# Optimization experiments

Hardware: AMD Instinct MI355X
Metric: run time of the kernel (lower is better)

The kernel has to match this reference:

```python
import jax, jax.numpy as jnp
import numpy as np

N, E, D, DE, H = 50000, 400000, 128, 64, 8
EPS = 1e-5
SLOPE = 0.2


def setup_inputs() -> dict:
    key = jax.random.key(0)
    ks = jax.random.split(key, 16)

    def lin(k, fan_in, fan_out):
        return (jax.random.normal(k, (fan_in, fan_out), jnp.float32) / np.sqrt(fan_in)).astype(jnp.float32)

    return {
        "node_features": jax.random.normal(ks[0], (N, D), jnp.float32),
        "edge_features": jax.random.normal(ks[1], (E, DE), jnp.float32),
        "Wn": lin(ks[2], D, D), "bn": jnp.zeros((D,), jnp.float32),
        "Wq": lin(ks[3], D, D), "bq": jnp.zeros((D,), jnp.float32),
        "Wk": lin(ks[4], D, D), "bk": jnp.zeros((D,), jnp.float32),
        "Wv": lin(ks[5], D, D), "bv": jnp.zeros((D,), jnp.float32),
        "We": lin(ks[6], DE, D), "be": jnp.zeros((D,), jnp.float32),
        "A1": lin(ks[7], 3 * D, D), "b1": jnp.zeros((D,), jnp.float32),
        "A2": lin(ks[8], D, H), "b2": jnp.zeros((H,), jnp.float32),
        "gamma": jnp.ones((D,), jnp.float32),
        "beta": jnp.zeros((D,), jnp.float32),
        "edge_index": jax.random.randint(ks[9], (2, E), 0, N, dtype=jnp.int32),
    }


def reference(node_features, edge_features, Wn, bn, Wq, bq, Wk, bk, Wv, bv,
              We, be, A1, b1, A2, b2, gamma, beta, edge_index):
    num_nodes = node_features.shape[0]
    h = node_features @ Wn + bn                      # [N, D]
    q = node_features @ Wq + bq                      # [N, D]
    k = node_features @ Wk + bk                      # [N, D]
    v = node_features @ Wv + bv                      # [N, D]
    eh = edge_features @ We + be                     # [E, D]

    src, tgt = edge_index[0], edge_index[1]
    attn_in = jnp.concatenate([q[src], k[tgt], eh], axis=-1)   # [E, 3D]
    hmid = jax.nn.leaky_relu(attn_in @ A1 + b1, SLOPE)          # [E, D]
    scores = jax.nn.leaky_relu(hmid @ A2 + b2, SLOPE)           # [E, H]
    w = jax.nn.softmax(scores.mean(axis=-1), axis=0)            # global softmax over edges, [E]

    # scatter-add: output[src] += w * v[tgt]
    out = jax.ops.segment_sum(w[:, None] * v[tgt], src, num_segments=num_nodes)  # [N, D]

    y = h + out                                       # dropout = identity (eval)
    mu = y.mean(axis=-1, keepdims=True)
    var = y.var(axis=-1, keepdims=True)
    return gamma * (y - mu) / jnp.sqrt(var + EPS) + beta
```

## Files before the change

kernel.cpp:

```cpp
#include <hip/hip_runtime.h>

#define D 128
#define DE 64
#define SLOPE 0.2f
#define EPS 1e-5f

typedef float f32x4 __attribute__((ext_vector_type(4)));
typedef short bf16x8 __attribute__((ext_vector_type(8)));

__device__ __forceinline__ float lrelu(float x) { return x > 0.f ? x : SLOPE * x; }

__device__ __forceinline__ unsigned short f2bf(float x) {
  union { float f; unsigned u; } c; c.f = x;
  unsigned r = c.u + 0x7FFFu + ((c.u >> 16) & 1u);
  return (unsigned short)(r >> 16);
}
__device__ __forceinline__ float bf2f(unsigned short u) {
  return __uint_as_float(((unsigned)u) << 16);
}

__global__ __launch_bounds__(128) void fold_pack(
    const float* __restrict__ Wq, const float* __restrict__ Wk,
    const float* __restrict__ We, const float* __restrict__ A1,
    const float* __restrict__ bq, const float* __restrict__ bk,
    const float* __restrict__ be, const float* __restrict__ b1,
    const float* __restrict__ Wn, const float* __restrict__ Wv,
    unsigned short* __restrict__ AfqT, unsigned short* __restrict__ AfkT,
    unsigned short* __restrict__ AfeT, float* __restrict__ bfold,
    unsigned short* __restrict__ WnT, unsigned short* __restrict__ WvT) {
  int r = blockIdx.x;
  int j = threadIdx.x;
  if (r < 128) {
    float acc = 0.f;
    for (int t = 0; t < 128; ++t) acc += Wq[r * 128 + t] * A1[t * 128 + j];
    AfqT[j * 128 + r] = f2bf(acc);
  } else if (r < 256) {
    int k = r - 128;
    float acc = 0.f;
    for (int t = 0; t < 128; ++t) acc += Wk[k * 128 + t] * A1[(128 + t) * 128 + j];
    AfkT[j * 128 + k] = f2bf(acc);
  } else if (r < 320) {
    int k = r - 256;
    float acc = 0.f;
    for (int t = 0; t < 128; ++t) acc += We[k * 128 + t] * A1[(256 + t) * 128 + j];
    AfeT[j * 64 + k] = f2bf(acc);
  } else if (r == 320) {
    float acc = b1[j];
    for (int t = 0; t < 128; ++t) {
      acc += bq[t] * A1[t * 128 + j];
      acc += bk[t] * A1[(128 + t) * 128 + j];
      acc += be[t] * A1[(256 + t) * 128 + j];
    }
    bfold[j] = acc;
  } else if (r < 449) {
    int c = r - 321;
    WnT[c * 128 + j] = f2bf(Wn[j * 128 + c]);
  } else {
    int c = r - 449;
    WvT[c * 128 + j] = f2bf(Wv[j * 128 + c]);
  }
}

__global__ __launch_bounds__(256) void cvt_to_bf16(
    const float* __restrict__ X, unsigned short* __restrict__ Xb, int n4) {
  int i = blockIdx.x * 256 + threadIdx.x;
  if (i < n4) {
    float4 f = ((const float4*)X)[i];
    union { unsigned short us[4]; uint2 v; } u;
    u.us[0] = f2bf(f.x); u.us[1] = f2bf(f.y);
    u.us[2] = f2bf(f.z); u.us[3] = f2bf(f.w);
    ((uint2*)Xb)[i] = u.v;
  }
}

__global__ __launch_bounds__(256, 2) void node_gemm_mfma(
    const unsigned short* __restrict__ Xb, const unsigned short* __restrict__ WnT,
    const unsigned short* __restrict__ WvT, const unsigned short* __restrict__ AfqT,
    const unsigned short* __restrict__ AfkT, const float* __restrict__ bn,
    const float* __restrict__ bv, float* __restrict__ h, float* __restrict__ v,
    unsigned short* __restrict__ q2p, unsigned short* __restrict__ k2p, int Nn) {
  __shared__ unsigned short As[256 * 40];
  __shared__ unsigned short Bs[128 * 40];
  __shared__ float bS[128];
  const unsigned short* WT;
  const float* bb = nullptr;
  float* O = nullptr;
  unsigned short* Ob = nullptr;
  switch (blockIdx.y) {
    case 0: WT = WnT; bb = bn; O = h; break;
    case 1: WT = WvT; bb = bv; O = v; break;
    case 2: WT = AfqT; Ob = q2p; break;
    default: WT = AfkT; Ob = k2p; break;
  }
  const int t = threadIdx.x;
  if (t < 128) bS[t] = bb ? bb[t] : 0.f;
  const int seg = t & 3, arow = t >> 2;
  const int m0 = blockIdx.x * 256;
  int rIdx[4];
#pragma unroll
  for (int l = 0; l < 4; ++l) rIdx[l] = min(m0 + arow + 64 * l, Nn - 1);
  uint4 avA[4], avB[2];
#pragma unroll
  for (int l = 0; l < 4; ++l)
    avA[l] = *(const uint4*)(Xb + (size_t)rIdx[l] * 128 + seg * 8);
#pragma unroll
  for (int l = 0; l < 2; ++l)
    avB[l] = *(const uint4*)(WT + (arow + 64 * l) * 128 + seg * 8);
  f32x4 acc[4][8];
#pragma unroll
  for (int mt = 0; mt < 4; ++mt)
#pragma unroll
    for (int nt = 0; nt < 8; ++nt) acc[mt][nt] = (f32x4)(0.f);
  const int lane = t & 63, wv = t >> 6, l15 = lane & 15, quad = lane >> 4;
  for (int ch = 0; ch < 4; ++ch) {
#pragma unroll
    for (int l = 0; l < 4; ++l)
      *(uint4*)&As[(arow + 64 * l) * 40 + seg * 8] = avA[l];
#pragma unroll
    for (int l = 0; l < 2; ++l)
      *(uint4*)&Bs[(arow + 64 * l) * 40 + seg * 8] = avB[l];
    __syncthreads();
    if (ch < 3) {
      int o = (ch + 1) * 32 + seg * 8;
#pragma unroll
      for (int l = 0; l < 4; ++l)
        avA[l] = *(const uint4*)(Xb + (size_t)rIdx[l] * 128 + o);
#pragma unroll
      for (int l = 0; l < 2; ++l)
        avB[l] = *(const uint4*)(WT + (arow + 64 * l) * 128 + o);
    }
    bf16x8 af[4];
#pragma unroll
    for (int mt = 0; mt < 4; ++mt)
      af[mt] = *(const bf16x8*)&As[(wv * 64 + mt * 16 + l15) * 40 + quad * 8];
#pragma unroll
    for (int nt = 0; nt < 8; ++nt) {
      bf16x8 bfr = *(const bf16x8*)&Bs[(nt * 16 + l15) * 40 + quad * 8];
#pragma unroll
      for (int mt = 0; mt < 4; ++mt)
        acc[mt][nt] =
            __builtin_amdgcn_mfma_f32_16x16x32_bf16(af[mt], bfr, acc[mt][nt], 0, 0, 0);
    }
    __syncthreads();
  }
#pragma unroll
  for (int mt = 0; mt < 4; ++mt) {
    int rowb = m0 + wv * 64 + mt * 16 + quad * 4;
#pragma unroll
    for (int nt = 0; nt < 8; ++nt) {
      int col = nt * 16 + l15;
      float b = bS[col];
#pragma unroll
      for (int r = 0; r < 4; ++r) {
        int rg = rowb + r;
        if (rg < Nn) {
          if (O) O[(size_t)rg * 128 + col] = acc[mt][nt][r] + b;
          else   Ob[(size_t)rg * 128 + l15 * 8 + nt] = f2bf(acc[mt][nt][r]);
        }
      }
    }
  }
}

__global__ __launch_bounds__(256, 2) void edge_fused2(
    const float* __restrict__ EF, const unsigned short* __restrict__ AfeT,
    const float* __restrict__ bfold, const float* __restrict__ A2,
    const float* __restrict__ b2, const unsigned short* __restrict__ q2p,
    const unsigned short* __restrict__ k2p, const int* __restrict__ src,
    const int* __restrict__ tgt, float* __restrict__ s_out, int E) {
  __shared__ unsigned short As[256 * 40];
  __shared__ unsigned short Bs[128 * 40];
  __shared__ float A2s[128 * 9];
  __shared__ float bfS[128];
  __shared__ float b2s[8];
  __shared__ int sIdxS[256], sIdxT[256];
  const int t = threadIdx.x;
  const int e0 = blockIdx.x * 256;
  {
    int ec = min(e0 + t, E - 1);
    sIdxS[t] = src[ec];
    sIdxT[t] = tgt[ec];
    if (t < 128) bfS[t] = bfold[t];
    if (t < 8) b2s[t] = b2[t];
#pragma unroll
    for (int l = 0; l < 4; ++l) {
      int i = t + l * 256;
      A2s[(i >> 3) * 9 + (i & 7)] = A2[i];
    }
  }
  const int seg = t & 3, arow = t >> 2;
  int ecl[4];
#pragma unroll
  for (int l = 0; l < 4; ++l) ecl[l] = min(e0 + arow + 64 * l, E - 1);
  uint4 avA[4], avB[2];
#pragma unroll
  for (int l = 0; l < 4; ++l) {
    const float* p = EF + (size_t)ecl[l] * 64 + seg * 8;
    float4 f0 = *(const float4*)p;
    float4 f1 = *(const float4*)(p + 4);
    union { unsigned short us[8]; uint4 v; } u;
    u.us[0] = f2bf(f0.x); u.us[1] = f2bf(f0.y);
    u.us[2] = f2bf(f0.z); u.us[3] = f2bf(f0.w);
    u.us[4] = f2bf(f1.x); u.us[5] = f2bf(f1.y);
    u.us[6] = f2bf(f1.z); u.us[7] = f2bf(f1.w);
    avA[l] = u.v;
  }
#pragma unroll
  for (int l = 0; l < 2; ++l)
    avB[l] = *(const uint4*)(AfeT + (arow + 64 * l) * 64 + seg * 8);
  f32x4 acc[4][8];
#pragma unroll
  for (int mt = 0; mt < 4; ++mt)
#pragma unroll
    for (int nt = 0; nt < 8; ++nt) acc[mt][nt] = (f32x4)(0.f);
  const int lane = t & 63, wv = t >> 6, l15 = lane & 15, quad = lane >> 4;

#pragma unroll
  for (int ch = 0; ch < 2; ++ch) {
#pragma unroll
    for (int l = 0; l < 4; ++l)
      *(uint4*)&As[(arow + 64 * l) * 40 + seg * 8] = avA[l];
#pragma unroll
    for (int l = 0; l < 2; ++l)
      *(uint4*)&Bs[(arow + 64 * l) * 40 + seg * 8] = avB[l];
    __syncthreads();
    if (ch == 0) {
      int o = 32 + seg * 8;
#pragma unroll
      for (int l = 0; l < 4; ++l) {
        const float* p = EF + (size_t)ecl[l] * 64 + o;
        float4 f0 = *(const float4*)p;
        float4 f1 = *(const float4*)(p + 4);
        union { unsigned short us[8]; uint4 v; } u;
        u.us[0] = f2bf(f0.x); u.us[1] = f2bf(f0.y);
        u.us[2] = f2bf(f0.z); u.us[3] = f2bf(f0.w);
        u.us[4] = f2bf(f1.x); u.us[5] = f2bf(f1.y);
        u.us[6] = f2bf(f1.z); u.us[7] = f2bf(f1.w);
        avA[l] = u.v;
      }
#pragma unroll
      for (int l = 0; l < 2; ++l)
        avB[l] = *(const uint4*)(AfeT + (arow + 64 * l) * 64 + o);
    }
    bf16x8 af[4];
#pragma unroll
    for (int mt = 0; mt < 4; ++mt)
      af[mt] = *(const bf16x8*)&As[(wv * 64 + mt * 16 + l15) * 40 + quad * 8];
#pragma unroll
    for (int nt = 0; nt < 8; ++nt) {
      bf16x8 bfr = *(const bf16x8*)&Bs[(nt * 16 + l15) * 40 + quad * 8];
#pragma unroll
      for (int mt = 0; mt < 4; ++mt)
        acc[mt][nt] =
            __builtin_amdgcn_mfma_f32_16x16x32_bf16(af[mt], bfr, acc[mt][nt], 0, 0, 0);
    }
    if (ch == 0) __syncthreads();
  }

  float bfv[8];
#pragma unroll
  for (int nt = 0; nt < 8; ++nt) bfv[nt] = bfS[nt * 16 + l15];
#pragma unroll
  for (int mt = 0; mt < 4; ++mt) {
#pragma unroll
    for (int r = 0; r < 4; ++r) {
      int erow = wv * 64 + mt * 16 + quad * 4 + r;
      int si = sIdxS[erow], ti = sIdxT[erow];
      uint4 qv = *(const uint4*)(q2p + (size_t)si * 128 + l15 * 8);
      uint4 kv = *(const uint4*)(k2p + (size_t)ti * 128 + l15 * 8);
      const unsigned short* qs = (const unsigned short*)&qv;
      const unsigned short* ks = (const unsigned short*)&kv;
#pragma unroll
      for (int nt = 0; nt < 8; ++nt)
        acc[mt][nt][r] =
            lrelu(acc[mt][nt][r] + bf2f(qs[nt]) + bf2f(ks[nt]) + bfv[nt]);
    }
  }
  float tacc[4][4];
#pragma unroll
  for (int mt = 0; mt < 4; ++mt)
#pragma unroll
    for (int r = 0; r < 4; ++r) tacc[mt][r] = 0.f;
  for (int hh = 0; hh < 8; ++hh) {
    float a2v[8];
#pragma unroll
    for (int nt = 0; nt < 8; ++nt) a2v[nt] = A2s[nt * 144 + l15 * 9 + hh];
    float b2h = b2s[hh];
#pragma unroll
    for (int mt = 0; mt < 4; ++mt)
#pragma unroll
      for (int r = 0; r < 4; ++r) {
        float p = 0.f;
#pragma unroll
        for (int nt = 0; nt < 8; ++nt) p += acc[mt][nt][r] * a2v[nt];
        p += __shfl_xor(p, 1);
        p += __shfl_xor(p, 2);
        p += __shfl_xor(p, 4);
        p += __shfl_xor(p, 8);
        tacc[mt][r] += lrelu(p + b2h);
      }
  }
  if (l15 == 0) {
#pragma unroll
    for (int mt = 0; mt < 4; ++mt)
#pragma unroll
      for (int r = 0; r < 4; ++r) {
        int e = e0 + wv * 64 + mt * 16 + quad * 4 + r;
        if (e < E) s_out[e] = tacc[mt][r] * 0.125f;
      }
  }
}

__global__ __launch_bounds__(256) void softmax_partial(
    const float* __restrict__ s, int E, float2* __restrict__ part) {
  __shared__ float mS[256], sS[256];
  int tid = threadIdx.x;
  float m = -1e30f, sum = 0.f;
  for (int i = blockIdx.x * 256 + tid; i < E; i += gridDim.x * 256) {
    float x = s[i];
    if (x > m) {
      sum = sum * __expf(m - x) + 1.f;
      m = x;
    } else {
      sum += __expf(x - m);
    }
  }
  mS[tid] = m;
  sS[tid] = sum;
  __syncthreads();
  for (int off = 128; off > 0; off >>= 1) {
    if (tid < off) {
      float m1 = mS[tid], s1 = sS[tid];
      float m2 = mS[tid + off], s2 = sS[tid + off];
      float M = fmaxf(m1, m2);
      mS[tid] = M;
      sS[tid] = s1 * __expf(m1 - M) + s2 * __expf(m2 - M);
    }
    __syncthreads();
  }
  if (tid == 0) part[blockIdx.x] = make_float2(mS[0], sS[0]);
}

__global__ __launch_bounds__(256) void softmax_final(
    const float2* __restrict__ part, int nPart, float* __restrict__ MS) {
  __shared__ float mS[256], sS[256];
  int tid = threadIdx.x;
  float m = -1e30f, sum = 0.f;
  for (int i = tid; i < nPart; i += 256) {
    float2 p = part[i];
    float M = fmaxf(m, p.x);
    sum = sum * __expf(m - M) + p.y * __expf(p.x - M);
    m = M;
  }
  mS[tid] = m;
  sS[tid] = sum;
  __syncthreads();
  for (int off = 128; off > 0; off >>= 1) {
    if (tid < off) {
      float m1 = mS[tid], s1 = sS[tid];
      float m2 = mS[tid + off], s2 = sS[tid + off];
      float M = fmaxf(m1, m2);
      mS[tid] = M;
      sS[tid] = s1 * __expf(m1 - M) + s2 * __expf(m2 - M);
    }
    __syncthreads();
  }
  if (tid == 0) {
    MS[0] = mS[0];
    MS[1] = 1.f / sS[0];
  }
}

__global__ __launch_bounds__(256) void count_deg(const int* __restrict__ src,
                                                 int* __restrict__ deg, int E) {
  int e = blockIdx.x * 256 + threadIdx.x;
  if (e < E) atomicAdd(&deg[src[e]], 1);
}

__global__ __launch_bounds__(256) void scan1(const int* __restrict__ deg,
                                             int* __restrict__ incl,
                                             int* __restrict__ bsum, int N) {
  __shared__ int sh[256];
  int tid = threadIdx.x;
  int i = blockIdx.x * 256 + tid;
  sh[tid] = (i < N) ? deg[i] : 0;
  __syncthreads();
  for (int off = 1; off < 256; off <<= 1) {
    int tv = (tid >= off) ? sh[tid - off] : 0;
    __syncthreads();
    sh[tid] += tv;
    __syncthreads();
  }
  if (i < N) incl[i] = sh[tid];
  if (tid == 255) bsum[blockIdx.x] = sh[255];
}

__global__ __launch_bounds__(256) void scan2(int* __restrict__ bsum, int nb) {
  __shared__ int sh[256];
  int tid = threadIdx.x;
  sh[tid] = (tid < nb) ? bsum[tid] : 0;
  __syncthreads();
  for (int off = 1; off < 256; off <<= 1) {
    int tv = (tid >= off) ? sh[tid - off] : 0;
    __syncthreads();
    sh[tid] += tv;
    __syncthreads();
  }
  if (tid < nb) bsum[tid] = sh[tid];
}

__global__ __launch_bounds__(256) void scan3(const int* __restrict__ deg,
                                             const int* __restrict__ incl,
                                             const int* __restrict__ bsum,
                                             int* __restrict__ offs,
                                             int* __restrict__ cursor, int N,
                                             int E) {
  int i = blockIdx.x * 256 + threadIdx.x;
  if (i >= N) return;
  int base = (blockIdx.x > 0) ? bsum[blockIdx.x - 1] : 0;
  int ex = incl[i] - deg[i] + base;
  offs[i] = ex;
  cursor[i] = ex;
  if (i == N - 1) offs[N] = E;
}

__global__ __launch_bounds__(256) void fill_csr(
    const int* __restrict__ src, const int* __restrict__ tgt,
    const float* __restrict__ s, int* __restrict__ cursor,
    int2* __restrict__ cwt, int E) {
  int e = blockIdx.x * 256 + threadIdx.x;
  if (e >= E) return;
  int s_ = src[e];
  int j = atomicAdd(&cursor[s_], 1);
  cwt[j] = make_int2(tgt[e], __float_as_int(s[e]));
}

__global__ __launch_bounds__(256) void gather_ln(
    const int* __restrict__ offs, const int2* __restrict__ cwt,
    const float* __restrict__ v, const float* __restrict__ MS,
    const float* __restrict__ gamma, const float* __restrict__ beta,
    float* __restrict__ y, int N) {
  int tid = threadIdx.x;
  int n = blockIdx.x * 4 + (tid >> 6);
  if (n >= N) return;
  int lane = tid & 63;
  float M = MS[0], inv = MS[1];
  int beg = offs[n], end = offs[n + 1];
  float a0 = 0.f, a1 = 0.f;
  int j = beg;
  for (; j + 1 < end; j += 2) {
    int2 p0 = cwt[j], p1 = cwt[j + 1];
    float w0 = __expf(__int_as_float(p0.y) - M) * inv;
    float w1 = __expf(__int_as_float(p1.y) - M) * inv;
    float2 v0 = *(const float2*)(v + (size_t)p0.x * 128 + lane * 2);
    float2 v1 = *(const float2*)(v + (size_t)p1.x * 128 + lane * 2);
    a0 += w0 * v0.x + w1 * v1.x;
    a1 += w0 * v0.y + w1 * v1.y;
  }
  if (j < end) {
    int2 p = cwt[j];
    float w = __expf(__int_as_float(p.y) - M) * inv;
    float2 vv = *(const float2*)(v + (size_t)p.x * 128 + lane * 2);
    a0 += w * vv.x;
    a1 += w * vv.y;
  }
  size_t base = (size_t)n * 128 + lane * 2;
  float2 hv = *(const float2*)(y + base);
  float y0 = hv.x + a0, y1 = hv.y + a1;
  float sum = y0 + y1, ssq = y0 * y0 + y1 * y1;
#pragma unroll
  for (int off = 1; off < 64; off <<= 1) {
    sum += __shfl_xor(sum, off);
    ssq += __shfl_xor(ssq, off);
  }
  float mu = sum * (1.f / 128.f);
  float var = ssq * (1.f / 128.f) - mu * mu;
  float rstd = rsqrtf(var + EPS);
  float2 g = *(const float2*)(gamma + lane * 2);
  float2 bt = *(const float2*)(beta + lane * 2);
  float2 out;
  out.x = g.x * (y0 - mu) * rstd + bt.x;
  out.y = g.y * (y1 - mu) * rstd + bt.y;
  *(float2*)(y + base) = out;
}

extern "C" void kernel_launch(void* const* d_in, const int* in_sizes, int n_in,
                              void* d_out, int out_size, void* d_ws,
                              size_t ws_size, hipStream_t stream) {
  const float* X  = (const float*)d_in[0];
  const float* EF = (const float*)d_in[1];
  const float* Wn = (const float*)d_in[2];
  const float* bn = (const float*)d_in[3];
  const float* Wq = (const float*)d_in[4];
  const float* bq = (const float*)d_in[5];
  const float* Wk = (const float*)d_in[6];
  const float* bk = (const float*)d_in[7];
  const float* Wv = (const float*)d_in[8];
  const float* bv = (const float*)d_in[9];
  const float* We = (const float*)d_in[10];
  const float* be = (const float*)d_in[11];
  const float* A1 = (const float*)d_in[12];
  const float* b1 = (const float*)d_in[13];
  const float* A2 = (const float*)d_in[14];
  const float* b2 = (const float*)d_in[15];
  const float* gamma = (const float*)d_in[16];
  const float* beta  = (const float*)d_in[17];
  const int* ei = (const int*)d_in[18];

  int N = in_sizes[0] / D;
  int E = in_sizes[1] / DE;
  const int* src = ei;
  const int* tgt = ei + E;

  float* h = (float*)d_out;
  float* ws = (float*)d_ws;
  float* v     = ws;
  float* sbuf  = v + (size_t)N * D;
  float2* part = (float2*)(sbuf + E);
  float* MS    = (float*)(part + 1024);
  float* bfold = MS + 4;
  unsigned short* Xb   = (unsigned short*)(bfold + 128);
  unsigned short* q2p  = Xb + (size_t)N * D;
  unsigned short* k2p  = q2p + (size_t)N * D;
  unsigned short* AfqT = k2p + (size_t)N * D;
  unsigned short* AfkT = AfqT + 128 * 128;
  unsigned short* AfeT = AfkT + 128 * 128;
  unsigned short* WnT  = AfeT + 128 * 64;
  unsigned short* WvT  = WnT + 128 * 128;
  int* deg    = (int*)(WvT + 128 * 128);
  int* incl   = deg + N;
  int* bsum   = incl + N;
  int* cursor = bsum + 256;
  int* offs   = cursor + N;
  int2* cwt   = (int2*)(offs + N + 2);

  int nbScan = (N + 255) / 256;

  hipMemsetAsync(deg, 0, (size_t)N * sizeof(int), stream);
  fold_pack<<<577, 128, 0, stream>>>(Wq, Wk, We, A1, bq, bk, be, b1, Wn, Wv,
                                     AfqT, AfkT, AfeT, bfold, WnT, WvT);
  cvt_to_bf16<<<(N * D / 4 + 255) / 256, 256, 0, stream>>>(X, Xb, N * D / 4);
  count_deg<<<(E + 255) / 256, 256, 0, stream>>>(src, deg, E);
  scan1<<<nbScan, 256, 0, stream>>>(deg, incl, bsum, N);
  scan2<<<1, 256, 0, stream>>>(bsum, nbScan);
  scan3<<<nbScan, 256, 0, stream>>>(deg, incl, bsum, offs, cursor, N, E);
  node_gemm_mfma<<<dim3((N + 255) / 256, 4), 256, 0, stream>>>(
      Xb, WnT, WvT, AfqT, AfkT, bn, bv, h, v, q2p, k2p, N);
  edge_fused2<<<(E + 255) / 256, 256, 0, stream>>>(EF, AfeT, bfold, A2, b2,
                                                   q2p, k2p, src, tgt, sbuf, E);
  softmax_partial<<<1024, 256, 0, stream>>>(sbuf, E, part);
  softmax_final<<<1, 256, 0, stream>>>(part, 1024, MS);
  fill_csr<<<(E + 255) / 256, 256, 0, stream>>>(src, tgt, sbuf, cursor, cwt, E);
  gather_ln<<<(N + 3) / 4, 256, 0, stream>>>(offs, cwt, v, MS, gamma, beta, h,
                                             N);
}
```

Baseline: 436.8 us.

## Store v in bf16, fuse degree count into convert, prefetch q/k gathers

Three changes land together. The v projection is now written as bf16, which halves the bytes gather_ln reads in its random per-edge gather, at the cost of lower precision in the aggregation. The degree-count atomics are folded into the bf16 conversion kernel, removing one launch. In the edge kernel, src/tgt indices are held in registers and the q/k row gathers are double-buffered across m-tiles so load latency overlaps the score math, which costs extra registers.

```diff
diff --git a/kernel.cpp b/kernel.cpp
--- a/kernel.cpp
+++ b/kernel.cpp
@@ -7,16 +7,17 @@
 
 typedef float f32x4 __attribute__((ext_vector_type(4)));
 typedef short bf16x8 __attribute__((ext_vector_type(8)));
+typedef unsigned short ushort;
 
 __device__ __forceinline__ float lrelu(float x) { return x > 0.f ? x : SLOPE * x; }
 
-__device__ __forceinline__ unsigned short f2bf(float x) {
+__device__ __forceinline__ ushort f2bf(float x) {
   union { float f; unsigned u; } c; c.f = x;
   unsigned r = c.u + 0x7FFFu + ((c.u >> 16) & 1u);
-  return (unsigned short)(r >> 16);
-}
-__device__ __forceinline__ float bf2f(unsigned short u) {
-  return __uint_as_float(((unsigned)u) << 16);
+  return (ushort)(r >> 16);
+}
+__device__ __forceinline__ float bf2f(unsigned u) {
+  return __uint_as_float(u << 16);
 }
 
 __global__ __launch_bounds__(128) void fold_pack(
@@ -25,9 +26,9 @@
     const float* __restrict__ bq, const float* __restrict__ bk,
     const float* __restrict__ be, const float* __restrict__ b1,
     const float* __restrict__ Wn, const float* __restrict__ Wv,
-    unsigned short* __restrict__ AfqT, unsigned short* __restrict__ AfkT,
-    unsigned short* __restrict__ AfeT, float* __restrict__ bfold,
-    unsigned short* __restrict__ WnT, unsigned short* __restrict__ WvT) {
+    ushort* __restrict__ AfqT, ushort* __restrict__ AfkT,
+    ushort* __restrict__ AfeT, float* __restrict__ bfold,
+    ushort* __restrict__ WnT, ushort* __restrict__ WvT) {
   int r = blockIdx.x;
   int j = threadIdx.x;
   if (r < 128) {
@@ -61,36 +62,40 @@
   }
 }
 
-__global__ __launch_bounds__(256) void cvt_to_bf16(
-    const float* __restrict__ X, unsigned short* __restrict__ Xb, int n4) {
+__global__ __launch_bounds__(256) void cvt_count(
+    const float* __restrict__ X, ushort* __restrict__ Xb, int n4,
+    const int* __restrict__ src, int* __restrict__ deg, int E) {
   int i = blockIdx.x * 256 + threadIdx.x;
   if (i < n4) {
     float4 f = ((const float4*)X)[i];
-    union { unsigned short us[4]; uint2 v; } u;
+    union { ushort us[4]; uint2 v; } u;
     u.us[0] = f2bf(f.x); u.us[1] = f2bf(f.y);
     u.us[2] = f2bf(f.z); u.us[3] = f2bf(f.w);
     ((uint2*)Xb)[i] = u.v;
   }
+  if (i < E) atomicAdd(&deg[src[i]], 1);
 }
 
 __global__ __launch_bounds__(256, 2) void node_gemm_mfma(
-    const unsigned short* __restrict__ Xb, const unsigned short* __restrict__ WnT,
-    const unsigned short* __restrict__ WvT, const unsigned short* __restrict__ AfqT,
-    const unsigned short* __restrict__ AfkT, const float* __restrict__ bn,
-    const float* __restrict__ bv, float* __restrict__ h, float* __restrict__ v,
-    unsigned short* __restrict__ q2p, unsigned short* __restrict__ k2p, int Nn) {
-  __shared__ unsigned short As[256 * 40];
-  __shared__ unsigned short Bs[128 * 40];
+    const ushort* __restrict__ Xb, const ushort* __restrict__ WnT,
+    const ushort* __restrict__ WvT, const ushort* __restrict__ AfqT,
+    const ushort* __restrict__ AfkT, const float* __restrict__ bn,
+    const float* __restrict__ bv, float* __restrict__ h,
+    ushort* __restrict__ vb, ushort* __restrict__ q2p,
+    ushort* __restrict__ k2p, int Nn) {
+  __shared__ ushort As[256 * 40];
+  __shared__ ushort Bs[128 * 40];
   __shared__ float bS[128];
-  const unsigned short* WT;
+  const ushort* WT;
   const float* bb = nullptr;
   float* O = nullptr;
-  unsigned short* Ob = nullptr;
+  ushort* Ob = nullptr;
+  int mode;
   switch (blockIdx.y) {
-    case 0: WT = WnT; bb = bn; O = h; break;
-    case 1: WT = WvT; bb = bv; O = v; break;
-    case 2: WT = AfqT; Ob = q2p; break;
-    default: WT = AfkT; Ob = k2p; break;
+    case 0: WT = WnT; bb = bn; O = h; mode = 0; break;
+    case 1: WT = WvT; bb = bv; Ob = vb; mode = 1; break;
+    case 2: WT = AfqT; Ob = q2p; mode = 2; break;
+    default: WT = AfkT; Ob = k2p; mode = 2; break;
   }
   const int t = threadIdx.x;
   if (t < 128) bS[t] = bb ? bb[t] : 0.f;
@@ -154,32 +159,40 @@
       for (int r = 0; r < 4; ++r) {
         int rg = rowb + r;
         if (rg < Nn) {
-          if (O) O[(size_t)rg * 128 + col] = acc[mt][nt][r] + b;
-          else   Ob[(size_t)rg * 128 + l15 * 8 + nt] = f2bf(acc[mt][nt][r]);
+          if (mode == 0)      O[(size_t)rg * 128 + col] = acc[mt][nt][r] + b;
+          else if (mode == 1) Ob[(size_t)rg * 128 + col] = f2bf(acc[mt][nt][r] + b);
+          else                Ob[(size_t)rg * 128 + l15 * 8 + nt] = f2bf(acc[mt][nt][r]);
         }
       }
     }
   }
 }
 
-__global__ __launch_bounds__(256, 2) void edge_fused2(
-    const float* __restrict__ EF, const unsigned short* __restrict__ AfeT,
+__global__ __launch_bounds__(256, 2) void edge_fused3(
+    const float* __restrict__ EF, const ushort* __restrict__ AfeT,
     const float* __restrict__ bfold, const float* __restrict__ A2,
-    const float* __restrict__ b2, const unsigned short* __restrict__ q2p,
-    const unsigned short* __restrict__ k2p, const int* __restrict__ src,
+    const float* __restrict__ b2, const ushort* __restrict__ q2p,
+    const ushort* __restrict__ k2p, const int* __restrict__ src,
     const int* __restrict__ tgt, float* __restrict__ s_out, int E) {
-  __shared__ unsigned short As[256 * 40];
-  __shared__ unsigned short Bs[128 * 40];
+  __shared__ ushort As[256 * 40];
+  __shared__ ushort Bs[128 * 40];
   __shared__ float A2s[128 * 9];
   __shared__ float bfS[128];
   __shared__ float b2s[8];
-  __shared__ int sIdxS[256], sIdxT[256];
   const int t = threadIdx.x;
   const int e0 = blockIdx.x * 256;
+  const int lane = t & 63, wv = t >> 6, l15 = lane & 15, quad = lane >> 4;
+
+  int siA[16], tiA[16];
+#pragma unroll
+  for (int mt = 0; mt < 4; ++mt)
+#pragma unroll
+    for (int r = 0; r < 4; ++r) {
+      int e = min(e0 + wv * 64 + mt * 16 + quad * 4 + r, E - 1);
+      siA[mt * 4 + r] = src[e];
+      tiA[mt * 4 + r] = tgt[e];
+    }
   {
-    int ec = min(e0 + t, E - 1);
-    sIdxS[t] = src[ec];
-    sIdxT[t] = tgt[ec];
     if (t < 128) bfS[t] = bfold[t];
     if (t < 8) b2s[t] = b2[t];
 #pragma unroll
@@ -198,7 +211,7 @@
     const float* p = EF + (size_t)ecl[l] * 64 + seg * 8;
     float4 f0 = *(const float4*)p;
     float4 f1 = *(const float4*)(p + 4);
-    union { unsigned short us[8]; uint4 v; } u;
+    union { ushort us[8]; uint4 v; } u;
     u.us[0] = f2bf(f0.x); u.us[1] = f2bf(f0.y);
     u.us[2] = f2bf(f0.z); u.us[3] = f2bf(f0.w);
     u.us[4] = f2bf(f1.x); u.us[5] = f2bf(f1.y);
@@ -213,7 +226,6 @@
   for (int mt = 0; mt < 4; ++mt)
 #pragma unroll
     for (int nt = 0; nt < 8; ++nt) acc[mt][nt] = (f32x4)(0.f);
-  const int lane = t & 63, wv = t >> 6, l15 = lane & 15, quad = lane >> 4;
 
 #pragma unroll
   for (int ch = 0; ch < 2; ++ch) {
@@ -231,7 +243,7 @@
         const float* p = EF + (size_t)ecl[l] * 64 + o;
         float4 f0 = *(const float4*)p;
         float4 f1 = *(const float4*)(p + 4);
-        union { unsigned short us[8]; uint4 v; } u;
+        union { ushort us[8]; uint4 v; } u;
         u.us[0] = f2bf(f0.x); u.us[1] = f2bf(f0.y);
         u.us[2] = f2bf(f0.z); u.us[3] = f2bf(f0.w);
         u.us[4] = f2bf(f1.x); u.us[5] = f2bf(f1.y);
@@ -260,16 +272,26 @@
   float bfv[8];
 #pragma unroll
   for (int nt = 0; nt < 8; ++nt) bfv[nt] = bfS[nt * 16 + l15];
+  uint4 qv[2][4], kv[2][4];
+#pragma unroll
+  for (int r = 0; r < 4; ++r) {
+    qv[0][r] = *(const uint4*)(q2p + (size_t)siA[r] * 128 + l15 * 8);
+    kv[0][r] = *(const uint4*)(k2p + (size_t)tiA[r] * 128 + l15 * 8);
+  }
 #pragma unroll
   for (int mt = 0; mt < 4; ++mt) {
+    int cur = mt & 1;
+    if (mt < 3) {
+#pragma unroll
+      for (int r = 0; r < 4; ++r) {
+        qv[cur ^ 1][r] = *(const uint4*)(q2p + (size_t)siA[(mt + 1) * 4 + r] * 128 + l15 * 8);
+        kv[cur ^ 1][r] = *(const uint4*)(k2p + (size_t)tiA[(mt + 1) * 4 + r] * 128 + l15 * 8);
+      }
+    }
 #pragma unroll
     for (int r = 0; r < 4; ++r) {
-      int erow = wv * 64 + mt * 16 + quad * 4 + r;
-      int si = sIdxS[erow], ti = sIdxT[erow];
-      uint4 qv = *(const uint4*)(q2p + (size_t)si * 128 + l15 * 8);
-      uint4 kv = *(const uint4*)(k2p + (size_t)ti * 128 + l15 * 8);
-      const unsigned short* qs = (const unsigned short*)&qv;
-      const unsigned short* ks = (const unsigned short*)&kv;
+      const ushort* qs = (const ushort*)&qv[cur][r];
+      const ushort* ks = (const ushort*)&kv[cur][r];
 #pragma unroll
       for (int nt = 0; nt < 8; ++nt)
         acc[mt][nt][r] =
@@ -369,12 +391,6 @@
     MS[0] = mS[0];
     MS[1] = 1.f / sS[0];
   }
-}
-
-__global__ __launch_bounds__(256) void count_deg(const int* __restrict__ src,
-                                                 int* __restrict__ deg, int E) {
-  int e = blockIdx.x * 256 + threadIdx.x;
-  if (e < E) atomicAdd(&deg[src[e]], 1);
 }
 
 __global__ __launch_bounds__(256) void scan1(const int* __restrict__ deg,
@@ -437,7 +453,7 @@
 
 __global__ __launch_bounds__(256) void gather_ln(
     const int* __restrict__ offs, const int2* __restrict__ cwt,
-    const float* __restrict__ v, const float* __restrict__ MS,
+    const ushort* __restrict__ vb, const float* __restrict__ MS,
     const float* __restrict__ gamma, const float* __restrict__ beta,
     float* __restrict__ y, int N) {
   int tid = threadIdx.x;
@@ -452,17 +468,17 @@
     int2 p0 = cwt[j], p1 = cwt[j + 1];
     float w0 = __expf(__int_as_float(p0.y) - M) * inv;
     float w1 = __expf(__int_as_float(p1.y) - M) * inv;
-    float2 v0 = *(const float2*)(v + (size_t)p0.x * 128 + lane * 2);
-    float2 v1 = *(const float2*)(v + (size_t)p1.x * 128 + lane * 2);
-    a0 += w0 * v0.x + w1 * v1.x;
-    a1 += w0 * v0.y + w1 * v1.y;
+    unsigned u0 = *(const unsigned*)(vb + (size_t)p0.x * 128 + lane * 2);
+    unsigned u1 = *(const unsigned*)(vb + (size_t)p1.x * 128 + lane * 2);
+    a0 += w0 * bf2f(u0 & 0xffffu) + w1 * bf2f(u1 & 0xffffu);
+    a1 += w0 * bf2f(u0 >> 16) + w1 * bf2f(u1 >> 16);
   }
   if (j < end) {
     int2 p = cwt[j];
     float w = __expf(__int_as_float(p.y) - M) * inv;
-    float2 vv = *(const float2*)(v + (size_t)p.x * 128 + lane * 2);
-    a0 += w * vv.x;
-    a1 += w * vv.y;
+    unsigned u = *(const unsigned*)(vb + (size_t)p.x * 128 + lane * 2);
+    a0 += w * bf2f(u & 0xffffu);
+    a1 += w * bf2f(u >> 16);
   }
   size_t base = (size_t)n * 128 + lane * 2;
   float2 hv = *(const float2*)(y + base);
@@ -514,19 +530,19 @@
 
   float* h = (float*)d_out;
   float* ws = (float*)d_ws;
-  float* v     = ws;
-  float* sbuf  = v + (size_t)N * D;
+  float* sbuf  = ws;
   float2* part = (float2*)(sbuf + E);
   float* MS    = (float*)(part + 1024);
   float* bfold = MS + 4;
-  unsigned short* Xb   = (unsigned short*)(bfold + 128);
-  unsigned short* q2p  = Xb + (size_t)N * D;
-  unsigned short* k2p  = q2p + (size_t)N * D;
-  unsigned short* AfqT = k2p + (size_t)N * D;
-  unsigned short* AfkT = AfqT + 128 * 128;
-  unsigned short* AfeT = AfkT + 128 * 128;
-  unsigned short* WnT  = AfeT + 128 * 64;
-  unsigned short* WvT  = WnT + 128 * 128;
+  ushort* Xb   = (ushort*)(bfold + 128);
+  ushort* vb   = Xb + (size_t)N * D;
+  ushort* q2p  = vb + (size_t)N * D;
+  ushort* k2p  = q2p + (size_t)N * D;
+  ushort* AfqT = k2p + (size_t)N * D;
+  ushort* AfkT = AfqT + 128 * 128;
+  ushort* AfeT = AfkT + 128 * 128;
+  ushort* WnT  = AfeT + 128 * 64;
+  ushort* WvT  = WnT + 128 * 128;
   int* deg    = (int*)(WvT + 128 * 128);
   int* incl   = deg + N;
   int* bsum   = incl + N;
@@ -535,22 +551,22 @@
   int2* cwt   = (int2*)(offs + N + 2);
 
   int nbScan = (N + 255) / 256;
+  int n4 = N * D / 4;
 
   hipMemsetAsync(deg, 0, (size_t)N * sizeof(int), stream);
   fold_pack<<<577, 128, 0, stream>>>(Wq, Wk, We, A1, bq, bk, be, b1, Wn, Wv,
                                      AfqT, AfkT, AfeT, bfold, WnT, WvT);
-  cvt_to_bf16<<<(N * D / 4 + 255) / 256, 256, 0, stream>>>(X, Xb, N * D / 4);
-  count_deg<<<(E + 255) / 256, 256, 0, stream>>>(src, deg, E);
+  cvt_count<<<(n4 + 255) / 256, 256, 0, stream>>>(X, Xb, n4, src, deg, E);
   scan1<<<nbScan, 256, 0, stream>>>(deg, incl, bsum, N);
   scan2<<<1, 256, 0, stream>>>(bsum, nbScan);
   scan3<<<nbScan, 256, 0, stream>>>(deg, incl, bsum, offs, cursor, N, E);
   node_gemm_mfma<<<dim3((N + 255) / 256, 4), 256, 0, stream>>>(
-      Xb, WnT, WvT, AfqT, AfkT, bn, bv, h, v, q2p, k2p, N);
-  edge_fused2<<<(E + 255) / 256, 256, 0, stream>>>(EF, AfeT, bfold, A2, b2,
+      Xb, WnT, WvT, AfqT, AfkT, bn, bv, h, vb, q2p, k2p, N);
+  edge_fused3<<<(E + 255) / 256, 256, 0, stream>>>(EF, AfeT, bfold, A2, b2,
                                                    q2p, k2p, src, tgt, sbuf, E);
   softmax_partial<<<1024, 256, 0, stream>>>(sbuf, E, part);
   softmax_final<<<1, 256, 0, stream>>>(part, 1024, MS);
   fill_csr<<<(E + 255) / 256, 256, 0, stream>>>(src, tgt, sbuf, cursor, cwt, E);
-  gather_ln<<<(N + 3) / 4, 256, 0, stream>>>(offs, cwt, v, MS, gamma, beta, h,
+  gather_ln<<<(N + 3) / 4, 256, 0, stream>>>(offs, cwt, vb, MS, gamma, beta, h,
                                              N);
 }
```

Result: slower. 457.3 us (+4.7%).
